# Kernel tuning notes

Hardware: AMD Instinct MI355X
Metric: run time of the kernel (lower is better)

The kernel has to match this reference:

```python
import jax, jax.numpy as jnp
from jax import lax
import numpy as np

B, T, N, C = 8, 12, 4000, 2
H, O = 64, 1


def setup_inputs() -> dict:
    key = jax.random.key(0)
    ks = jax.random.split(key, 10)
    s = 1.0 / np.sqrt(H)
    return {
        "x": jax.random.normal(ks[0], (B, T, N, C), jnp.float32),
        "adj": jax.random.uniform(ks[1], (N, N), jnp.float32) / N,  # row-normalized-ish
        "W_gcn": jax.random.normal(ks[2], (H, C), jnp.float32) * s,
        "b_gcn": jax.random.normal(ks[3], (H,), jnp.float32) * s,
        "W_ih": jax.random.normal(ks[4], (4 * H, H), jnp.float32) * s,
        "W_hh": jax.random.normal(ks[5], (4 * H, H), jnp.float32) * s,
        "b_ih": jax.random.normal(ks[6], (4 * H,), jnp.float32) * s,
        "b_hh": jax.random.normal(ks[7], (4 * H,), jnp.float32) * s,
        "W_out": jax.random.normal(ks[8], (O, H), jnp.float32) * s,
        "b_out": jax.random.normal(ks[9], (O,), jnp.float32) * s,
    }


def reference(x, adj, W_gcn, b_gcn, W_ih, W_hh, b_ih, b_hh, W_out, b_out):
    b, t, n, c = x.shape
    h_dim = W_hh.shape[1]
    # per-timestep graph aggregation + shared linear GCN + relu (all timesteps batched)
    xg = jnp.einsum('nm,btmc->btnc', adj, x)          # [B,T,N,C]
    g = jax.nn.relu(xg @ W_gcn.T + b_gcn)             # [B,T,N,H]
    # shared LSTM applied per node == one LSTM over flattened batch B*N
    seq = g.transpose(1, 0, 2, 3).reshape(t, b * n, h_dim)  # [T, B*N, H]

    def step(carry, xt):
        h, cst = carry
        gates = xt @ W_ih.T + b_ih + h @ W_hh.T + b_hh  # [B*N, 4H]
        i, f, gg, o = jnp.split(gates, 4, axis=-1)      # torch gate order i,f,g,o
        cst = jax.nn.sigmoid(f) * cst + jax.nn.sigmoid(i) * jnp.tanh(gg)
        h = jax.nn.sigmoid(o) * jnp.tanh(cst)
        return (h, cst), None

    init = (jnp.zeros((b * n, h_dim), x.dtype), jnp.zeros((b * n, h_dim), x.dtype))
    (h_last, _), _ = lax.scan(step, init, seq)
    h_last = h_last.reshape(b, n, h_dim)              # [B,N,H]
    return h_last @ W_out.T + b_out                   # [B,N,O]
```

## Files before the change

### kernel.cpp

```cpp
#include <hip/hip_runtime.h>

typedef _Float16 half8 __attribute__((ext_vector_type(8)));
typedef short short8v __attribute__((ext_vector_type(8)));
typedef float floatx4 __attribute__((ext_vector_type(4)));

#define GLOBAL_AS __attribute__((address_space(1)))
#define LDS_AS __attribute__((address_space(3)))

__device__ __forceinline__ unsigned short f2bf(float f) {
  unsigned int u = __float_as_uint(f);
  unsigned int r = (u + 0x7FFFu + ((u >> 16) & 1u)) >> 16;
  return (unsigned short)r;
}
__device__ __forceinline__ float sigf(float x) {
  return __builtin_amdgcn_rcpf(1.f + __expf(-x));
}
__device__ __forceinline__ float tanhf_(float x) {
  return 1.f - 2.f * __builtin_amdgcn_rcpf(1.f + __expf(2.f * x));
}

__global__ __launch_bounds__(256) void prep_kernel(
    const float* __restrict__ x, const float* __restrict__ W_ih,
    const float* __restrict__ W_hh, unsigned short* __restrict__ XBT,
    unsigned short* __restrict__ Wt2) {
  int idx = blockIdx.x * 256 + threadIdx.x;
  if (idx < 192 * 4032) {
    int j = idx / 4032;
    int m = idx - j * 4032;
    unsigned short v = 0;
    if (m < 4000) {
      int b = j / 24, r = j - b * 24;
      int t = r >> 1, c = r & 1;
      v = f2bf(x[((b * 12 + t) * 4000 + m) * 2 + c]);
    }
    XBT[idx] = v;
  } else {
    int widx = idx - 192 * 4032;
    int j = widx >> 7, k = widx & 127;
    float val = (k < 64) ? W_ih[j * 64 + k] : W_hh[j * 64 + (k - 64)];
    _Float16 h = (_Float16)val;
    Wt2[widx] = __builtin_bit_cast(unsigned short, h);
  }
}

__global__ __launch_bounds__(256, 2) void gcn_gemm_kernel(
    const float* __restrict__ adj, const unsigned short* __restrict__ XBT,
    float* __restrict__ XGT) {
  __shared__ float Ab[2][1024];
  __shared__ unsigned short Bb[2][12288];
  int tid = threadIdx.x;
  int w = tid >> 6, lane = tid & 63, l15 = lane & 15, kg = lane >> 4;
  int n0 = blockIdx.x * 16;

  int a_row = (w << 2) + (lane >> 4);
  int a_g = lane & 15;
  int a_gx = (a_g & 8) | ((a_g ^ a_row) & 7);
  const float* aSrc = adj + (size_t)(n0 + a_row) * 4000 + (a_gx << 2);
  const float* aSrcT = adj + (size_t)(n0 + a_row) * 4000 + 3968 +
                       ((a_g < 8) ? (((a_g ^ a_row) & 7) << 2) : 0);
  const unsigned short* bSrc[6];
  int bj[6];
#pragma unroll
  for (int q = 0; q < 6; q++) {
    int ib = w * 6 + q;
    int j = ib * 8 + (lane >> 3);
    int g = lane & 7;
    bj[q] = ib * 512;
    bSrc[q] = XBT + (size_t)j * 4032 + ((g ^ (j & 7)) << 3);
  }

#define STAGE_K2(kt, buf)                                                      \
  {                                                                            \
    __builtin_amdgcn_global_load_lds((const GLOBAL_AS unsigned int*)(aSrc + (kt)), \
        (LDS_AS unsigned int*)&Ab[(buf)][w * 256], 16, 0, 0);                  \
    _Pragma("unroll")                                                          \
    for (int q = 0; q < 6; q++)                                                \
      __builtin_amdgcn_global_load_lds((const GLOBAL_AS unsigned int*)(bSrc[q] + (kt)), \
          (LDS_AS unsigned int*)&Bb[(buf)][bj[q]], 16, 0, 0);                  \
  }
#define STAGE_K2T(buf)                                                         \
  {                                                                            \
    __builtin_amdgcn_global_load_lds((const GLOBAL_AS unsigned int*)(aSrcT),   \
        (LDS_AS unsigned int*)&Ab[(buf)][w * 256], 16, 0, 0);                  \
    _Pragma("unroll")                                                          \
    for (int q = 0; q < 6; q++)                                                \
      __builtin_amdgcn_global_load_lds((const GLOBAL_AS unsigned int*)(bSrc[q] + 3968), \
          (LDS_AS unsigned int*)&Bb[(buf)][bj[q]], 16, 0, 0);                  \
  }

  floatx4 acc[3];
  acc[0] = acc[1] = acc[2] = floatx4{0.f, 0.f, 0.f, 0.f};
  int rowA = l15;
  int xA = (rowA & 7) << 2;
  int jb[3], xB[3];
#pragma unroll
  for (int ct = 0; ct < 3; ct++) {
    int j = w * 48 + ct * 16 + l15;
    jb[ct] = j * 64;
    xB[ct] = (j & 7) << 3;
  }

  STAGE_K2(0, 0);
  for (int i = 0; i < 62; i++) {
    int cur = i & 1;
    if (i < 61) { STAGE_K2((i + 1) * 64, cur ^ 1); }
    else        { STAGE_K2T(cur ^ 1); }
    asm volatile("s_waitcnt vmcnt(7)" ::: "memory");
    __builtin_amdgcn_s_barrier();
    asm volatile("" ::: "memory");
#pragma unroll
    for (int ks = 0; ks < 2; ks++) {
      int k0 = ks * 32 + kg * 8;
      float4 u = *reinterpret_cast<const float4*>(&Ab[cur][rowA * 64 + (k0 ^ xA)]);
      float4 v = *reinterpret_cast<const float4*>(&Ab[cur][rowA * 64 + ((k0 + 4) ^ xA)]);
      short8v af;
      af[0] = f2bf(u.x); af[1] = f2bf(u.y); af[2] = f2bf(u.z); af[3] = f2bf(u.w);
      af[4] = f2bf(v.x); af[5] = f2bf(v.y); af[6] = f2bf(v.z); af[7] = f2bf(v.w);
#pragma unroll
      for (int ct = 0; ct < 3; ct++) {
        short8v bf = *reinterpret_cast<const short8v*>(&Bb[cur][jb[ct] + (k0 ^ xB[ct])]);
        acc[ct] = __builtin_amdgcn_mfma_f32_16x16x32_bf16(af, bf, acc[ct], 0, 0, 0);
      }
    }
    __builtin_amdgcn_s_barrier();
  }
  asm volatile("s_waitcnt vmcnt(0)" ::: "memory");
  __builtin_amdgcn_s_barrier();
  asm volatile("" ::: "memory");
  {
    int k0 = kg * 8;
    float4 u = *reinterpret_cast<const float4*>(&Ab[0][rowA * 64 + (k0 ^ xA)]);
    float4 v = *reinterpret_cast<const float4*>(&Ab[0][rowA * 64 + ((k0 + 4) ^ xA)]);
    short8v af;
    af[0] = f2bf(u.x); af[1] = f2bf(u.y); af[2] = f2bf(u.z); af[3] = f2bf(u.w);
    af[4] = f2bf(v.x); af[5] = f2bf(v.y); af[6] = f2bf(v.z); af[7] = f2bf(v.w);
#pragma unroll
    for (int ct = 0; ct < 3; ct++) {
      short8v bf = *reinterpret_cast<const short8v*>(&Bb[0][jb[ct] + (k0 ^ xB[ct])]);
      acc[ct] = __builtin_amdgcn_mfma_f32_16x16x32_bf16(af, bf, acc[ct], 0, 0, 0);
    }
  }
#pragma unroll
  for (int ct = 0; ct < 3; ct++) {
    int j = w * 48 + ct * 16 + l15;
#pragma unroll
    for (int e = 0; e < 4; e++) {
      int n = n0 + kg * 4 + e;
      XGT[(size_t)j * 4000 + n] = acc[ct][e];
    }
  }
}

__global__ __launch_bounds__(256, 3) void lstm_kernel(
    const float* __restrict__ XGT, const unsigned short* __restrict__ Wt2,
    const float* __restrict__ W_gcn, const float* __restrict__ b_gcn,
    const float* __restrict__ b_ih, const float* __restrict__ b_hh,
    const float* __restrict__ W_out, const float* __restrict__ b_out,
    float* __restrict__ out) {
  __shared__ unsigned short A[32 * 128];
  __shared__ float xga[24 * 32];
  __shared__ float red[8 * 32];

  int tid = threadIdx.x;
  int w = tid >> 6, lane = tid & 63, l15 = lane & 15, kg = lane >> 4;
  int r0 = blockIdx.x * 32;
  int hidx = w * 16 + l15;

  half8 wf[4][4];
#pragma unroll
  for (int ct = 0; ct < 4; ct++) {
    int j = ct * 64 + hidx;
#pragma unroll
    for (int ks = 0; ks < 4; ks++)
      wf[ct][ks] = *reinterpret_cast<const half8*>(&Wt2[j * 128 + ks * 32 + kg * 8]);
  }
  float bI = b_ih[hidx] + b_hh[hidx];
  float bF = b_ih[64 + hidx] + b_hh[64 + hidx];
  float bG = b_ih[128 + hidx] + b_hh[128 + hidx];
  float bO = b_ih[192 + hidx] + b_hh[192 + hidx];
  float wg0 = W_gcn[2 * hidx], wg1 = W_gcn[2 * hidx + 1], bg = b_gcn[hidx];

  for (int i = tid; i < 32 * 128 / 2; i += 256)
    reinterpret_cast<unsigned int*>(A)[i] = 0u;
  for (int i = tid; i < 24 * 32; i += 256) {
    int row = i & 31, tc = i >> 5;
    int g = r0 + row;
    int b = g / 4000, n = g - b * 4000;
    xga[i] = XGT[(size_t)(b * 24 + tc) * 4000 + n];
  }
  float creg[8];
#pragma unroll
  for (int i = 0; i < 8; i++) creg[i] = 0.f;
  __syncthreads();

  for (int t = 0; t < 12; t++) {
#pragma unroll
    for (int half = 0; half < 2; half++)
#pragma unroll
      for (int rr = 0; rr < 4; rr++) {
        int row = half * 16 + kg * 4 + rr;
        float xg0 = xga[(2 * t) * 32 + row];
        float xg1 = xga[(2 * t + 1) * 32 + row];
        float gv = fmaxf(xg0 * wg0 + xg1 * wg1 + bg, 0.f);
        _Float16 hv = (_Float16)gv;
        A[row * 128 + (hidx ^ ((row & 7) << 3))] = __builtin_bit_cast(unsigned short, hv);
      }
    __syncthreads();

    floatx4 acc[2][4];
#pragma unroll
    for (int rt = 0; rt < 2; rt++)
#pragma unroll
      for (int ct = 0; ct < 4; ct++) acc[rt][ct] = floatx4{0.f, 0.f, 0.f, 0.f};
#pragma unroll
    for (int rt = 0; rt < 2; rt++) {
      int row = rt * 16 + l15;
      int xr = (row & 7) << 3;
      half8 af[4];
#pragma unroll
      for (int ks = 0; ks < 4; ks++)
        af[ks] = *reinterpret_cast<const half8*>(&A[row * 128 + ((ks * 32 + kg * 8) ^ xr)]);
#pragma unroll
      for (int ks = 0; ks < 4; ks++)
#pragma unroll
        for (int ct = 0; ct < 4; ct++)
          acc[rt][ct] = __builtin_amdgcn_mfma_f32_16x16x32_f16(
              af[ks], wf[ct][ks], acc[rt][ct], 0, 0, 0);
    }
    __syncthreads();

#pragma unroll
    for (int rt = 0; rt < 2; rt++)
#pragma unroll
      for (int e = 0; e < 4; e++) {
        int row = rt * 16 + kg * 4 + e;
        float gi = acc[rt][0][e] + bI;
        float gf = acc[rt][1][e] + bF;
        float gg = acc[rt][2][e] + bG;
        float go = acc[rt][3][e] + bO;
        float c = sigf(gf) * creg[rt * 4 + e] + sigf(gi) * tanhf_(gg);
        creg[rt * 4 + e] = c;
        float h = sigf(go) * tanhf_(c);
        _Float16 hv = (_Float16)h;
        A[row * 128 + ((64 + hidx) ^ ((row & 7) << 3))] = __builtin_bit_cast(unsigned short, hv);
      }
  }
  __syncthreads();

  {
    int rg = tid & 31, kq = tid >> 5;
    float partial = 0.f;
#pragma unroll
    for (int i = 0; i < 8; i++) {
      int k = kq * 8 + i;
      float hv = (float)__builtin_bit_cast(
          _Float16, A[rg * 128 + ((64 + k) ^ ((rg & 7) << 3))]);
      partial += hv * W_out[k];
    }
    red[kq * 32 + rg] = partial;
  }
  __syncthreads();
  if (tid < 32) {
    float s = b_out[0];
#pragma unroll
    for (int i = 0; i < 8; i++) s += red[i * 32 + tid];
    out[r0 + tid] = s;
  }
}

extern "C" void kernel_launch(void* const* d_in, const int* in_sizes, int n_in,
                              void* d_out, int out_size, void* d_ws, size_t ws_size,
                              hipStream_t stream) {
  const float* x     = (const float*)d_in[0];
  const float* adj   = (const float*)d_in[1];
  const float* W_gcn = (const float*)d_in[2];
  const float* b_gcn = (const float*)d_in[3];
  const float* W_ih  = (const float*)d_in[4];
  const float* W_hh  = (const float*)d_in[5];
  const float* b_ih  = (const float*)d_in[6];
  const float* b_hh  = (const float*)d_in[7];
  const float* W_out = (const float*)d_in[8];
  const float* b_out = (const float*)d_in[9];
  float* outp = (float*)d_out;

  float* XGT = (float*)d_ws;
  unsigned short* XBT = (unsigned short*)((char*)d_ws + 3072000);
  unsigned short* Wt2 = (unsigned short*)((char*)d_ws + 4620288);

  prep_kernel<<<3152, 256, 0, stream>>>(x, W_ih, W_hh, XBT, Wt2);
  gcn_gemm_kernel<<<250, 256, 0, stream>>>(adj, XBT, XGT);
  lstm_kernel<<<1000, 256, 0, stream>>>(XGT, Wt2, W_gcn, b_gcn, b_ih, b_hh,
                                        W_out, b_out, outp);
}
```

Baseline: 215.9 us.

## Split-K the adjacency GEMM into 7 chunks and vectorize prep kernel

The GCN aggregation GEMM previously ran only 250 blocks across the whole K=4000 range. It now splits K into 7 chunks of 9 tiles, launching 1750 blocks that each write partial sums to a larger workspace. The LSTM kernel then adds the 7 partials when it loads its inputs. Separately, the prep kernel is vectorized to process 4 nodes and 8 weights per thread with wide loads and stores. This trades extra partial-sum traffic for much better CU occupancy on the memory-bound adjacency read.

```diff
diff --git a/kernel.cpp b/kernel.cpp
--- a/kernel.cpp
+++ b/kernel.cpp
@@ -2,6 +2,7 @@
 
 typedef _Float16 half8 __attribute__((ext_vector_type(8)));
 typedef short short8v __attribute__((ext_vector_type(8)));
+typedef unsigned short ushort4v __attribute__((ext_vector_type(4)));
 typedef float floatx4 __attribute__((ext_vector_type(4)));
 
 #define GLOBAL_AS __attribute__((address_space(1)))
@@ -24,33 +25,50 @@
     const float* __restrict__ W_hh, unsigned short* __restrict__ XBT,
     unsigned short* __restrict__ Wt2) {
   int idx = blockIdx.x * 256 + threadIdx.x;
-  if (idx < 192 * 4032) {
-    int j = idx / 4032;
-    int m = idx - j * 4032;
-    unsigned short v = 0;
-    if (m < 4000) {
-      int b = j / 24, r = j - b * 24;
-      int t = r >> 1, c = r & 1;
-      v = f2bf(x[((b * 12 + t) * 4000 + m) * 2 + c]);
-    }
-    XBT[idx] = v;
+  if (idx < 96 * 1008) {
+    int bt = idx / 1008;
+    int mg = idx - bt * 1008;
+    int m0 = mg * 4;
+    int j0 = bt * 2;
+    ushort4v c0, c1;
+    if (m0 < 4000) {
+      const float* px = x + ((size_t)bt * 4000 + m0) * 2;
+      float4 v0 = *reinterpret_cast<const float4*>(px);
+      float4 v1 = *reinterpret_cast<const float4*>(px + 4);
+      c0[0] = f2bf(v0.x); c0[1] = f2bf(v0.z); c0[2] = f2bf(v1.x); c0[3] = f2bf(v1.z);
+      c1[0] = f2bf(v0.y); c1[1] = f2bf(v0.w); c1[2] = f2bf(v1.y); c1[3] = f2bf(v1.w);
+    } else {
+      c0 = ushort4v{0, 0, 0, 0};
+      c1 = ushort4v{0, 0, 0, 0};
+    }
+    *reinterpret_cast<ushort4v*>(&XBT[(size_t)j0 * 4032 + m0]) = c0;
+    *reinterpret_cast<ushort4v*>(&XBT[(size_t)(j0 + 1) * 4032 + m0]) = c1;
   } else {
-    int widx = idx - 192 * 4032;
-    int j = widx >> 7, k = widx & 127;
-    float val = (k < 64) ? W_ih[j * 64 + k] : W_hh[j * 64 + (k - 64)];
-    _Float16 h = (_Float16)val;
-    Wt2[widx] = __builtin_bit_cast(unsigned short, h);
+    int widx = idx - 96 * 1008;
+    int j = widx >> 4, kq = widx & 15;
+    const float* src = (kq < 8) ? (W_ih + j * 64 + kq * 8)
+                                : (W_hh + j * 64 + (kq - 8) * 8);
+    float4 v0 = *reinterpret_cast<const float4*>(src);
+    float4 v1 = *reinterpret_cast<const float4*>(src + 4);
+    half8 h;
+    h[0] = (_Float16)v0.x; h[1] = (_Float16)v0.y; h[2] = (_Float16)v0.z; h[3] = (_Float16)v0.w;
+    h[4] = (_Float16)v1.x; h[5] = (_Float16)v1.y; h[6] = (_Float16)v1.z; h[7] = (_Float16)v1.w;
+    *reinterpret_cast<half8*>(&Wt2[j * 128 + kq * 8]) = h;
   }
 }
 
 __global__ __launch_bounds__(256, 2) void gcn_gemm_kernel(
     const float* __restrict__ adj, const unsigned short* __restrict__ XBT,
-    float* __restrict__ XGT) {
+    float* __restrict__ XGP) {
   __shared__ float Ab[2][1024];
   __shared__ unsigned short Bb[2][12288];
   int tid = threadIdx.x;
   int w = tid >> 6, lane = tid & 63, l15 = lane & 15, kg = lane >> 4;
-  int n0 = blockIdx.x * 16;
+  int bid = blockIdx.x;
+  int ch = bid / 250;
+  int nb = bid - ch * 250;
+  int n0 = nb * 16;
+  int k0 = ch * 576;
 
   int a_row = (w << 2) + (lane >> 4);
   int a_g = lane & 15;
@@ -100,59 +118,48 @@
     xB[ct] = (j & 7) << 3;
   }
 
-  STAGE_K2(0, 0);
-  for (int i = 0; i < 62; i++) {
+  STAGE_K2(k0, 0);
+  for (int i = 0; i < 9; i++) {
     int cur = i & 1;
-    if (i < 61) { STAGE_K2((i + 1) * 64, cur ^ 1); }
-    else        { STAGE_K2T(cur ^ 1); }
-    asm volatile("s_waitcnt vmcnt(7)" ::: "memory");
+    int gtile = ch * 9 + i;
+    if (i < 8) {
+      if (ch * 9 + i + 1 == 62) { STAGE_K2T(cur ^ 1); }
+      else                      { STAGE_K2(k0 + (i + 1) * 64, cur ^ 1); }
+      asm volatile("s_waitcnt vmcnt(7)" ::: "memory");
+    } else {
+      asm volatile("s_waitcnt vmcnt(0)" ::: "memory");
+    }
     __builtin_amdgcn_s_barrier();
     asm volatile("" ::: "memory");
-#pragma unroll
-    for (int ks = 0; ks < 2; ks++) {
-      int k0 = ks * 32 + kg * 8;
-      float4 u = *reinterpret_cast<const float4*>(&Ab[cur][rowA * 64 + (k0 ^ xA)]);
-      float4 v = *reinterpret_cast<const float4*>(&Ab[cur][rowA * 64 + ((k0 + 4) ^ xA)]);
+    int kslim = (gtile == 62) ? 1 : 2;
+    for (int ks = 0; ks < kslim; ks++) {
+      int k0i = ks * 32 + kg * 8;
+      float4 u = *reinterpret_cast<const float4*>(&Ab[cur][rowA * 64 + (k0i ^ xA)]);
+      float4 v = *reinterpret_cast<const float4*>(&Ab[cur][rowA * 64 + ((k0i + 4) ^ xA)]);
       short8v af;
       af[0] = f2bf(u.x); af[1] = f2bf(u.y); af[2] = f2bf(u.z); af[3] = f2bf(u.w);
       af[4] = f2bf(v.x); af[5] = f2bf(v.y); af[6] = f2bf(v.z); af[7] = f2bf(v.w);
 #pragma unroll
       for (int ct = 0; ct < 3; ct++) {
-        short8v bf = *reinterpret_cast<const short8v*>(&Bb[cur][jb[ct] + (k0 ^ xB[ct])]);
+        short8v bf = *reinterpret_cast<const short8v*>(&Bb[cur][jb[ct] + (k0i ^ xB[ct])]);
         acc[ct] = __builtin_amdgcn_mfma_f32_16x16x32_bf16(af, bf, acc[ct], 0, 0, 0);
       }
     }
     __builtin_amdgcn_s_barrier();
   }
-  asm volatile("s_waitcnt vmcnt(0)" ::: "memory");
-  __builtin_amdgcn_s_barrier();
-  asm volatile("" ::: "memory");
-  {
-    int k0 = kg * 8;
-    float4 u = *reinterpret_cast<const float4*>(&Ab[0][rowA * 64 + (k0 ^ xA)]);
-    float4 v = *reinterpret_cast<const float4*>(&Ab[0][rowA * 64 + ((k0 + 4) ^ xA)]);
-    short8v af;
-    af[0] = f2bf(u.x); af[1] = f2bf(u.y); af[2] = f2bf(u.z); af[3] = f2bf(u.w);
-    af[4] = f2bf(v.x); af[5] = f2bf(v.y); af[6] = f2bf(v.z); af[7] = f2bf(v.w);
-#pragma unroll
-    for (int ct = 0; ct < 3; ct++) {
-      short8v bf = *reinterpret_cast<const short8v*>(&Bb[0][jb[ct] + (k0 ^ xB[ct])]);
-      acc[ct] = __builtin_amdgcn_mfma_f32_16x16x32_bf16(af, bf, acc[ct], 0, 0, 0);
-    }
-  }
 #pragma unroll
   for (int ct = 0; ct < 3; ct++) {
     int j = w * 48 + ct * 16 + l15;
 #pragma unroll
     for (int e = 0; e < 4; e++) {
       int n = n0 + kg * 4 + e;
-      XGT[(size_t)j * 4000 + n] = acc[ct][e];
+      XGP[(size_t)ch * 768000 + (size_t)j * 4000 + n] = acc[ct][e];
     }
   }
 }
 
 __global__ __launch_bounds__(256, 3) void lstm_kernel(
-    const float* __restrict__ XGT, const unsigned short* __restrict__ Wt2,
+    const float* __restrict__ XGP, const unsigned short* __restrict__ Wt2,
     const float* __restrict__ W_gcn, const float* __restrict__ b_gcn,
     const float* __restrict__ b_ih, const float* __restrict__ b_hh,
     const float* __restrict__ W_out, const float* __restrict__ b_out,
@@ -186,7 +193,11 @@
     int row = i & 31, tc = i >> 5;
     int g = r0 + row;
     int b = g / 4000, n = g - b * 4000;
-    xga[i] = XGT[(size_t)(b * 24 + tc) * 4000 + n];
+    size_t base = (size_t)(b * 24 + tc) * 4000 + n;
+    float s = 0.f;
+#pragma unroll
+    for (int chh = 0; chh < 7; chh++) s += XGP[(size_t)chh * 768000 + base];
+    xga[i] = s;
   }
   float creg[8];
 #pragma unroll
@@ -283,12 +294,12 @@
   const float* b_out = (const float*)d_in[9];
   float* outp = (float*)d_out;
 
-  float* XGT = (float*)d_ws;
-  unsigned short* XBT = (unsigned short*)((char*)d_ws + 3072000);
-  unsigned short* Wt2 = (unsigned short*)((char*)d_ws + 4620288);
-
-  prep_kernel<<<3152, 256, 0, stream>>>(x, W_ih, W_hh, XBT, Wt2);
-  gcn_gemm_kernel<<<250, 256, 0, stream>>>(adj, XBT, XGT);
-  lstm_kernel<<<1000, 256, 0, stream>>>(XGT, Wt2, W_gcn, b_gcn, b_ih, b_hh,
+  float* XGP = (float*)d_ws;
+  unsigned short* XBT = (unsigned short*)((char*)d_ws + 21504000);
+  unsigned short* Wt2 = (unsigned short*)((char*)d_ws + 23052288);
+
+  prep_kernel<<<394, 256, 0, stream>>>(x, W_ih, W_hh, XBT, Wt2);
+  gcn_gemm_kernel<<<1750, 256, 0, stream>>>(adj, XBT, XGP);
+  lstm_kernel<<<1000, 256, 0, stream>>>(XGP, Wt2, W_gcn, b_gcn, b_ih, b_hh,
                                         W_out, b_out, outp);
 }
```

Measured after the change: 195.9 us. 9.2% less time.
